# Kernel tuning notes

Hardware: AMD Instinct MI355X
Metric: run time of the kernel (lower is better)

## Reference

```python
import jax, jax.numpy as jnp
import numpy as np

L, B, S, D, H = 4, 4, 2048, 512, 8
DH = D // H
FF = 4 * D
BN_EPS = 1e-3  # keras BatchNormalization default epsilon


def setup_inputs() -> dict:
    key = jax.random.key(0)
    ks = jax.random.split(key, 8)
    g = lambda k, shape: jax.random.normal(k, shape, dtype=jnp.float32) * 0.02
    return {
        "sequence": jax.random.normal(ks[0], (B, S, D), dtype=jnp.float32),
        "wq": g(ks[1], (L, D, D)), "bq": jnp.zeros((L, D), jnp.float32),
        "wk": g(ks[2], (L, D, D)), "bk": jnp.zeros((L, D), jnp.float32),
        "wv": g(ks[3], (L, D, D)), "bv": jnp.zeros((L, D), jnp.float32),
        "wo": g(ks[4], (L, D, D)), "bo": jnp.zeros((L, D), jnp.float32),
        "w1": g(ks[5], (L, D, FF)), "b1": jnp.zeros((L, FF), jnp.float32),
        "w2": g(ks[6], (L, FF, D)), "b2": jnp.zeros((L, D), jnp.float32),
        "g1": jnp.ones((L, D), jnp.float32), "be1": jnp.zeros((L, D), jnp.float32),
        "g2": jnp.ones((L, D), jnp.float32), "be2": jnp.zeros((L, D), jnp.float32),
    }


def reference(sequence, wq, bq, wk, bk, wv, bv, wo, bo, w1, b1, w2, b2, g1, be1, g2, be2):
    # Inference-mode BatchNorm with moving_mean=0, moving_var=1:
    # bn(x) = x / sqrt(1 + eps) * gamma + beta
    bn_inv = 1.0 / jnp.sqrt(jnp.float32(1.0 + BN_EPS))
    scale = 1.0 / jnp.sqrt(jnp.float32(DH))
    x = sequence  # [B, S, D]
    for i in range(L):
        # Batched multi-head self-attention (== the per-position loop concat)
        q = (x @ wq[i] + bq[i]).reshape(B, S, H, DH)
        k = (x @ wk[i] + bk[i]).reshape(B, S, H, DH)
        v = (x @ wv[i] + bv[i]).reshape(B, S, H, DH)
        att = jax.nn.softmax(jnp.einsum('bqhd,bkhd->bhqk', q, k) * scale, axis=-1)
        o = jnp.einsum('bhqk,bkhd->bqhd', att, v).reshape(B, S, D)
        o = o @ wo[i] + bo[i]
        x = (x + o) * bn_inv * g1[i] + be1[i]          # residual + BN
        f = jax.nn.relu(x @ w1[i] + b1[i]) @ w2[i] + b2[i]  # FFN
        x = (x + f) * bn_inv * g2[i] + be2[i]          # residual + BN
    return x
```

## Files before the change

kernel.cpp:

```cpp
#include <hip/hip_runtime.h>
#include <hip/hip_bf16.h>

#define BB   4
#define SS   2048
#define DDIM 512
#define HH   8
#define DHD  64
#define FFD  2048
#define LLN  4
#define NQKV 1536
#define BN_INV 0.9995003747f
#define QSCALE 0.18033688011112042f

typedef __bf16 bf16x8 __attribute__((ext_vector_type(8)));
typedef __bf16 bf16x4 __attribute__((ext_vector_type(4)));
typedef float  f32x4  __attribute__((ext_vector_type(4)));

__device__ __forceinline__ void gl2lds16(const void* g, void* l) {
  __builtin_amdgcn_global_load_lds((const __attribute__((address_space(1))) void*)g,
                                   (__attribute__((address_space(3))) void*)l, 16, 0, 0);
}

__global__ __launch_bounds__(256) void k_transpose_w(const float* __restrict__ in,
                                                     __bf16* __restrict__ out,
                                                     int R, int C,
                                                     size_t in_zs, size_t out_zs) {
  __shared__ float tile[32][33];
  in += (size_t)blockIdx.z * in_zs;
  out += (size_t)blockIdx.z * out_zs;
  const int c0 = blockIdx.x * 32, r0 = blockIdx.y * 32;
  const int tx = threadIdx.x & 31, ty = threadIdx.x >> 5;
#pragma unroll
  for (int k = 0; k < 4; ++k) {
    int r = ty + k * 8;
    tile[r][tx] = in[(size_t)(r0 + r) * C + (c0 + tx)];
  }
  __syncthreads();
#pragma unroll
  for (int k = 0; k < 4; ++k) {
    int c = ty + k * 8;
    out[(size_t)(c0 + c) * R + (r0 + tx)] = (__bf16)tile[tx][c];
  }
}

__global__ __launch_bounds__(256) void k_bias_fuse(const float* __restrict__ bq,
                                                   const float* __restrict__ bk,
                                                   const float* __restrict__ bv,
                                                   float* __restrict__ out) {
  const int i = blockIdx.x * 256 + threadIdx.x;
  const int l = i / NQKV, j = i - l * NQKV;
  float v = (j < 512) ? bq[l * 512 + j]
          : (j < 1024) ? bk[l * 512 + j - 512]
                       : bv[l * 512 + j - 1024];
  out[i] = v;
}

__global__ __launch_bounds__(256) void k_transpose_v(const __bf16* __restrict__ qkv,
                                                     __bf16* __restrict__ vt) {
  __shared__ __bf16 tile[32][33];
  const int s0 = blockIdx.x * 32;
  const int d0 = blockIdx.y * 32;
  const int bh = blockIdx.z, b = bh >> 3, h = bh & 7;
  const int tx = threadIdx.x & 31, ty = threadIdx.x >> 5;
#pragma unroll
  for (int k = 0; k < 4; ++k) {
    int s = ty + k * 8;
    tile[s][tx] = qkv[(size_t)(b * SS + s0 + s) * NQKV + 2 * DDIM + h * DHD + d0 + tx];
  }
  __syncthreads();
#pragma unroll
  for (int k = 0; k < 4; ++k) {
    int d = ty + k * 8;
    vt[(size_t)(bh * DHD + d0 + d) * SS + (s0 + tx)] = tile[tx][d];
  }
}

__global__ __launch_bounds__(256) void k_cast(const float* __restrict__ in,
                                              float* __restrict__ xf,
                                              __bf16* __restrict__ xb) {
  const int i = (blockIdx.x * 256 + threadIdx.x) * 4;
  const float4 v = *(const float4*)(in + i);
  *(float4*)(xf + i) = v;
  bf16x4 o;
  o[0] = (__bf16)v.x; o[1] = (__bf16)v.y; o[2] = (__bf16)v.z; o[3] = (__bf16)v.w;
  *(bf16x4*)(xb + i) = o;
}

template <int EPI>
__global__ __launch_bounds__(256) void k_gemm_bt(const __bf16* __restrict__ A,
                                                 const __bf16* __restrict__ Bt,
                                                 const float* __restrict__ bias,
                                                 __bf16* __restrict__ Cb,
                                                 int M, int N, int K,
                                                 const float* __restrict__ xres,
                                                 float* __restrict__ xout,
                                                 const float* __restrict__ gvec,
                                                 const float* __restrict__ bvec) {
  __shared__ char As[2][16384];
  __shared__ char Bs[2][16384];
  const int tid = threadIdx.x;
  const int l = tid & 63, w = tid >> 6;
  const int wm = w >> 1, wn = w & 1;
  const int m0 = blockIdx.y * 128, n0 = blockIdx.x * 128;
  const int lr = l & 15, lg = l >> 4;
  f32x4 acc[4][4] = {};
  const int nk = K >> 6;
  const size_t ldab = (size_t)K * 2;

  auto stage = [&](int buf, int kt) {
    const int k0b = kt * 128;
#pragma unroll
    for (int i = 0; i < 4; ++i) {
      const int chunk = i * 256 + tid;
      const int row = chunk >> 3;
      const int scb = ((chunk & 7) * 16) ^ ((row & 7) << 4);
      gl2lds16((const char*)A + (size_t)(m0 + row) * ldab + k0b + scb,
               As[buf] + (i * 256 + w * 64) * 16);
      gl2lds16((const char*)Bt + (size_t)(n0 + row) * ldab + k0b + scb,
               Bs[buf] + (i * 256 + w * 64) * 16);
    }
  };

  stage(0, 0);
  __syncthreads();
  int cur = 0;
  for (int kt = 0; kt < nk; ++kt) {
    if (kt + 1 < nk) stage(cur ^ 1, kt + 1);
#pragma unroll
    for (int kk = 0; kk < 2; ++kk) {
      bf16x8 a[4], b[4];
#pragma unroll
      for (int m = 0; m < 4; ++m) {
        const int row = wm * 64 + m * 16 + lr;
        const int cb = kk * 64 + lg * 16;
        a[m] = *(const bf16x8*)(As[cur] + row * 128 + (cb ^ ((row & 7) << 4)));
      }
#pragma unroll
      for (int n = 0; n < 4; ++n) {
        const int row = wn * 64 + n * 16 + lr;
        const int cb = kk * 64 + lg * 16;
        b[n] = *(const bf16x8*)(Bs[cur] + row * 128 + (cb ^ ((row & 7) << 4)));
      }
#pragma unroll
      for (int m = 0; m < 4; ++m)
#pragma unroll
        for (int n = 0; n < 4; ++n)
          acc[m][n] = __builtin_amdgcn_mfma_f32_16x16x32_bf16(a[m], b[n], acc[m][n], 0, 0, 0);
    }
    asm volatile("s_waitcnt vmcnt(0)" ::: "memory");
    __syncthreads();
    cur ^= 1;
  }
#pragma unroll
  for (int m = 0; m < 4; ++m) {
    const int gm = m0 + wm * 64 + m * 16 + lg * 4;
#pragma unroll
    for (int n = 0; n < 4; ++n) {
      const int gn = n0 + wn * 64 + n * 16 + lr;
      const float bv_ = bias[gn];
#pragma unroll
      for (int j = 0; j < 4; ++j) {
        const size_t idx = (size_t)(gm + j) * N + gn;
        float v = acc[m][n][j] + bv_;
        if constexpr (EPI == 1) {
          Cb[idx] = (__bf16)fmaxf(v, 0.0f);
        } else if constexpr (EPI == 2) {
          float t = (xres[idx] + v) * BN_INV * gvec[gn] + bvec[gn];
          xout[idx] = t;
          Cb[idx] = (__bf16)t;
        } else {
          if (gn < DDIM) v *= QSCALE;
          Cb[idx] = (__bf16)v;
        }
      }
    }
  }
}

__global__ __launch_bounds__(512, 4) void k_attn(const __bf16* __restrict__ QKV,
                                                 const __bf16* __restrict__ Vt,
                                                 __bf16* __restrict__ O) {
  __shared__ char smem[81920];
  const int tid = threadIdx.x, l = tid & 63, w = tid >> 6;
  const int lr = l & 15, lg = l >> 4;
  const int f = blockIdx.y * 16 + blockIdx.x;
  const int L = (f & 7) * 64 + (f >> 3);
  const int qt = L & 15, bh = L >> 4;
  const int b = bh >> 3, h = bh & 7;
  const int q0 = qt * 128 + w * 16;
  bf16x8 aq[2];
  {
    const __bf16* qp = QKV + (size_t)(b * SS + q0 + lr) * NQKV + h * DHD + lg * 8;
    aq[0] = *(const bf16x8*)qp;
    aq[1] = *(const bf16x8*)(qp + 32);
  }
  f32x4 oacc[4] = {};
  float rsum[4] = {0.f, 0.f, 0.f, 0.f};
  char* pw = smem + 65536 + w * 2048;

  auto stage = [&](int buf, int t) {
    const int kv0 = t * 128;
    char* Kd = smem + buf * 16384;
    char* Vd = smem + 32768 + buf * 16384;
#pragma unroll
    for (int i = 0; i < 2; ++i) {
      const int chunk = i * 512 + tid;
      const int row = chunk >> 3;
      const int scb = ((chunk & 7) * 16) ^ ((row & 7) << 4);
      gl2lds16((const char*)QKV + ((size_t)(b * SS + kv0 + row) * NQKV + DDIM + h * DHD) * 2 + scb,
               Kd + (i * 512 + w * 64) * 16);
    }
#pragma unroll
    for (int i = 0; i < 2; ++i) {
      const int chunk = i * 512 + tid;
      const int row = chunk >> 4;
      const int scb = ((chunk & 15) * 16) ^ ((row & 7) << 4);
      gl2lds16((const char*)Vt + ((size_t)(bh * DHD + row) * SS + kv0) * 2 + scb,
               Vd + (i * 512 + w * 64) * 16);
    }
  };

  stage(0, 0);
  __syncthreads();
  int cur = 0;
  for (int t = 0; t < SS / 128; ++t) {
    if (t < SS / 128 - 1) stage(cur ^ 1, t + 1);
    const char* Ks = smem + cur * 16384;
    const char* Vs = smem + 32768 + cur * 16384;
    f32x4 s[8];
    __builtin_amdgcn_s_setprio(1);
#pragma unroll
    for (int n = 0; n < 8; ++n) {
      const int row = n * 16 + lr;
      const int swz = (row & 7) << 4;
      bf16x8 kf0 = *(const bf16x8*)(Ks + row * 128 + ((lg * 16) ^ swz));
      bf16x8 kf1 = *(const bf16x8*)(Ks + row * 128 + ((64 + lg * 16) ^ swz));
      f32x4 z = {};
      z = __builtin_amdgcn_mfma_f32_16x16x32_bf16(aq[0], kf0, z, 0, 0, 0);
      z = __builtin_amdgcn_mfma_f32_16x16x32_bf16(aq[1], kf1, z, 0, 0, 0);
      s[n] = z;
    }
    __builtin_amdgcn_s_setprio(0);
#pragma unroll
    for (int hv = 0; hv < 2; ++hv) {
#pragma unroll
      for (int nn = 0; nn < 4; ++nn)
#pragma unroll
        for (int j = 0; j < 4; ++j) {
          const float p = __builtin_amdgcn_exp2f(s[hv * 4 + nn][j]);
          rsum[j] += p;
          const int r = lg * 4 + j;
          const int cb = (nn * 16 + lr) * 2;
          *(__bf16*)(pw + r * 128 + (cb ^ ((r & 7) << 4))) = (__bf16)p;
        }
      __builtin_amdgcn_s_setprio(1);
#pragma unroll
      for (int kk2 = 0; kk2 < 2; ++kk2) {
        const int kkg = hv * 2 + kk2;
        const bf16x8 ap = *(const bf16x8*)(pw + lr * 128 + ((kk2 * 64 + lg * 16) ^ ((lr & 7) << 4)));
#pragma unroll
        for (int n = 0; n < 4; ++n) {
          const int row = n * 16 + lr;
          bf16x8 vf = *(const bf16x8*)(Vs + row * 256 + ((kkg * 64 + lg * 16) ^ ((row & 7) << 4)));
          oacc[n] = __builtin_amdgcn_mfma_f32_16x16x32_bf16(ap, vf, oacc[n], 0, 0, 0);
        }
      }
      __builtin_amdgcn_s_setprio(0);
    }
    asm volatile("s_waitcnt vmcnt(0)" ::: "memory");
    __syncthreads();
    cur ^= 1;
  }
#pragma unroll
  for (int j = 0; j < 4; ++j) {
    float v = rsum[j];
    v += __shfl_xor(v, 1);
    v += __shfl_xor(v, 2);
    v += __shfl_xor(v, 4);
    v += __shfl_xor(v, 8);
    const float inv = 1.0f / v;
    const int sr = q0 + lg * 4 + j;
#pragma unroll
    for (int n = 0; n < 4; ++n)
      O[(size_t)(b * SS + sr) * DDIM + h * DHD + n * 16 + lr] = (__bf16)(oacc[n][j] * inv);
  }
}

static constexpr size_t SZ_WQKVT = (size_t)LLN * NQKV * DDIM * 2;
static constexpr size_t SZ_WOT   = (size_t)LLN * DDIM * DDIM * 2;
static constexpr size_t SZ_WT_DF = (size_t)LLN * DDIM * FFD * 2;
static constexpr size_t SZ_BQKV  = (size_t)LLN * NQKV * 4;
static constexpr size_t SZ_X     = (size_t)BB * SS * DDIM * 4;
static constexpr size_t SZ_ABF   = (size_t)BB * SS * DDIM * 2;
static constexpr size_t SZ_QKV   = (size_t)BB * SS * NQKV * 2;
static constexpr size_t OFF_WQKVT = 0;
static constexpr size_t OFF_WOT  = OFF_WQKVT + SZ_WQKVT;
static constexpr size_t OFF_W1T  = OFF_WOT + SZ_WOT;
static constexpr size_t OFF_W2T  = OFF_W1T + SZ_WT_DF;
static constexpr size_t OFF_BQKV = OFF_W2T + SZ_WT_DF;
static constexpr size_t OFF_X    = OFF_BQKV + SZ_BQKV;
static constexpr size_t OFF_XB   = OFF_X + SZ_X;
static constexpr size_t OFF_QKV  = OFF_XB + SZ_ABF;
static constexpr size_t OFF_VT   = OFF_QKV + SZ_QKV;
static constexpr size_t OFF_OB   = OFF_VT + SZ_ABF;
static constexpr size_t OFF_H1   = OFF_QKV;

extern "C" void kernel_launch(void* const* d_in, const int* in_sizes, int n_in,
                              void* d_out, int out_size, void* d_ws, size_t ws_size,
                              hipStream_t stream) {
  const float* seq = (const float*)d_in[0];
  const float* wq = (const float*)d_in[1];  const float* bq = (const float*)d_in[2];
  const float* wk = (const float*)d_in[3];  const float* bk = (const float*)d_in[4];
  const float* wv = (const float*)d_in[5];  const float* bv = (const float*)d_in[6];
  const float* wo = (const float*)d_in[7];  const float* bo = (const float*)d_in[8];
  const float* w1 = (const float*)d_in[9];  const float* b1 = (const float*)d_in[10];
  const float* w2 = (const float*)d_in[11]; const float* b2 = (const float*)d_in[12];
  const float* g1 = (const float*)d_in[13]; const float* be1 = (const float*)d_in[14];
  const float* g2 = (const float*)d_in[15]; const float* be2 = (const float*)d_in[16];

  char* ws = (char*)d_ws;
  __bf16* wqkvt = (__bf16*)(ws + OFF_WQKVT);
  __bf16* wot = (__bf16*)(ws + OFF_WOT);
  __bf16* w1t = (__bf16*)(ws + OFF_W1T);
  __bf16* w2t = (__bf16*)(ws + OFF_W2T);
  float*  bqkv = (float*)(ws + OFF_BQKV);
  float*  xf  = (float*)(ws + OFF_X);
  __bf16* xb  = (__bf16*)(ws + OFF_XB);
  __bf16* qkvb = (__bf16*)(ws + OFF_QKV);
  __bf16* vtb = (__bf16*)(ws + OFF_VT);
  __bf16* ob  = (__bf16*)(ws + OFF_OB);
  __bf16* h1  = (__bf16*)(ws + OFF_H1);

  const size_t zDD = (size_t)DDIM * DDIM;
  const size_t zQKV = (size_t)NQKV * DDIM;
  const size_t zDF = (size_t)DDIM * FFD;
  k_transpose_w<<<dim3(16, 16, LLN), 256, 0, stream>>>(wq, wqkvt, DDIM, DDIM, zDD, zQKV);
  k_transpose_w<<<dim3(16, 16, LLN), 256, 0, stream>>>(wk, wqkvt + (size_t)DDIM * DDIM, DDIM, DDIM, zDD, zQKV);
  k_transpose_w<<<dim3(16, 16, LLN), 256, 0, stream>>>(wv, wqkvt + (size_t)2 * DDIM * DDIM, DDIM, DDIM, zDD, zQKV);
  k_transpose_w<<<dim3(16, 16, LLN), 256, 0, stream>>>(wo, wot, DDIM, DDIM, zDD, zDD);
  k_transpose_w<<<dim3(64, 16, LLN), 256, 0, stream>>>(w1, w1t, DDIM, FFD, zDF, zDF);
  k_transpose_w<<<dim3(16, 64, LLN), 256, 0, stream>>>(w2, w2t, FFD, DDIM, zDF, zDF);
  k_bias_fuse<<<LLN * NQKV / 256, 256, 0, stream>>>(bq, bk, bv, bqkv);
  k_cast<<<4096, 256, 0, stream>>>(seq, xf, xb);

  const int M = BB * SS;
  for (int i = 0; i < LLN; ++i) {
    k_gemm_bt<3><<<dim3(NQKV / 128, M / 128), 256, 0, stream>>>(
        xb, wqkvt + (size_t)i * NQKV * DDIM, bqkv + i * NQKV, qkvb, M, NQKV, DDIM,
        nullptr, nullptr, nullptr, nullptr);
    k_transpose_v<<<dim3(SS / 32, DHD / 32, BB * HH), 256, 0, stream>>>(qkvb, vtb);
    k_attn<<<dim3(SS / 128, BB * HH), 512, 0, stream>>>(qkvb, vtb, ob);
    k_gemm_bt<2><<<dim3(DDIM / 128, M / 128), 256, 0, stream>>>(
        ob, wot + (size_t)i * DDIM * DDIM, bo + i * DDIM, xb, M, DDIM, DDIM,
        xf, xf, g1 + i * DDIM, be1 + i * DDIM);
    k_gemm_bt<1><<<dim3(FFD / 128, M / 128), 256, 0, stream>>>(
        xb, w1t + (size_t)i * DDIM * FFD, b1 + i * FFD, h1, M, FFD, DDIM,
        nullptr, nullptr, nullptr, nullptr);
    k_gemm_bt<2><<<dim3(DDIM / 128, M / 128), 256, 0, stream>>>(
        h1, w2t + (size_t)i * DDIM * FFD, b2 + i * DDIM, xb, M, DDIM, FFD,
        xf, (i == LLN - 1) ? (float*)d_out : xf, g2 + i * DDIM, be2 + i * DDIM);
  }
  (void)in_sizes; (void)n_in; (void)out_size; (void)ws_size;
}
```

Before: 677.1 us.

## Restructure attention to 32x32 MFMA computing S^T so P stays in registers

Rewrites the attention kernel to use 32x32x16 bf16 MFMAs with 4 waves of 32 query rows each, computing the transposed score tile so that the exponentiated probabilities land directly in the B-operand layout for the PV MFMA. This removes the per-wave LDS round trip for P, along with its shared memory and barriers, and shrinks the block to 256 threads. K rows are permuted during staging and the V swizzle is widened to match the new fragment layout. The risks are lower occupancy from fewer waves per block and higher register pressure from the 16-wide accumulators, plus the correctness of the new row permutation.

Measured after the change: 642.5 us. 5.1% less time.

```diff
diff --git a/kernel.cpp b/kernel.cpp
--- a/kernel.cpp
+++ b/kernel.cpp
@@ -15,10 +15,17 @@
 typedef __bf16 bf16x8 __attribute__((ext_vector_type(8)));
 typedef __bf16 bf16x4 __attribute__((ext_vector_type(4)));
 typedef float  f32x4  __attribute__((ext_vector_type(4)));
+typedef float  f32x16 __attribute__((ext_vector_type(16)));
 
 __device__ __forceinline__ void gl2lds16(const void* g, void* l) {
   __builtin_amdgcn_global_load_lds((const __attribute__((address_space(1))) void*)g,
                                    (__attribute__((address_space(3))) void*)l, 16, 0, 0);
+}
+
+__device__ __forceinline__ unsigned pkbf16(float a, float b) {
+  union { __bf16 h[2]; unsigned u; } x;
+  x.h[0] = (__bf16)a; x.h[1] = (__bf16)b;
+  return x.u;
 }
 
 __global__ __launch_bounds__(256) void k_transpose_w(const float* __restrict__ in,
@@ -177,46 +184,47 @@
   }
 }
 
-__global__ __launch_bounds__(512, 4) void k_attn(const __bf16* __restrict__ QKV,
+__global__ __launch_bounds__(256, 2) void k_attn(const __bf16* __restrict__ QKV,
                                                  const __bf16* __restrict__ Vt,
                                                  __bf16* __restrict__ O) {
-  __shared__ char smem[81920];
+  __shared__ char smem[65536];
   const int tid = threadIdx.x, l = tid & 63, w = tid >> 6;
-  const int lr = l & 15, lg = l >> 4;
+  const int lq = l & 31, hi = l >> 5;
   const int f = blockIdx.y * 16 + blockIdx.x;
   const int L = (f & 7) * 64 + (f >> 3);
   const int qt = L & 15, bh = L >> 4;
   const int b = bh >> 3, h = bh & 7;
-  const int q0 = qt * 128 + w * 16;
-  bf16x8 aq[2];
+  const int myq = qt * 128 + w * 32 + lq;
+  bf16x8 qf[4];
   {
-    const __bf16* qp = QKV + (size_t)(b * SS + q0 + lr) * NQKV + h * DHD + lg * 8;
-    aq[0] = *(const bf16x8*)qp;
-    aq[1] = *(const bf16x8*)(qp + 32);
-  }
-  f32x4 oacc[4] = {};
-  float rsum[4] = {0.f, 0.f, 0.f, 0.f};
-  char* pw = smem + 65536 + w * 2048;
+    const __bf16* qp = QKV + (size_t)(b * SS + myq) * NQKV + h * DHD + hi * 8;
+#pragma unroll
+    for (int kc = 0; kc < 4; ++kc)
+      qf[kc] = *(const bf16x8*)(qp + kc * 16);
+  }
+  f32x16 oaccT[2] = {};
+  float rsum = 0.f;
 
   auto stage = [&](int buf, int t) {
     const int kv0 = t * 128;
     char* Kd = smem + buf * 16384;
     char* Vd = smem + 32768 + buf * 16384;
 #pragma unroll
-    for (int i = 0; i < 2; ++i) {
-      const int chunk = i * 512 + tid;
+    for (int i = 0; i < 4; ++i) {
+      const int chunk = i * 256 + tid;
       const int row = chunk >> 3;
+      const int rs = row ^ ((((row >> 2) + 1) & 2) * 6);
       const int scb = ((chunk & 7) * 16) ^ ((row & 7) << 4);
-      gl2lds16((const char*)QKV + ((size_t)(b * SS + kv0 + row) * NQKV + DDIM + h * DHD) * 2 + scb,
-               Kd + (i * 512 + w * 64) * 16);
-    }
-#pragma unroll
-    for (int i = 0; i < 2; ++i) {
-      const int chunk = i * 512 + tid;
+      gl2lds16((const char*)QKV + ((size_t)(b * SS + kv0 + rs) * NQKV + DDIM + h * DHD) * 2 + scb,
+               Kd + (i * 256 + w * 64) * 16);
+    }
+#pragma unroll
+    for (int i = 0; i < 4; ++i) {
+      const int chunk = i * 256 + tid;
       const int row = chunk >> 4;
-      const int scb = ((chunk & 15) * 16) ^ ((row & 7) << 4);
+      const int scb = ((chunk & 15) * 16) ^ ((row & 15) << 4);
       gl2lds16((const char*)Vt + ((size_t)(bh * DHD + row) * SS + kv0) * 2 + scb,
-               Vd + (i * 512 + w * 64) * 16);
+               Vd + (i * 256 + w * 64) * 16);
     }
   };
 
@@ -227,43 +235,38 @@
     if (t < SS / 128 - 1) stage(cur ^ 1, t + 1);
     const char* Ks = smem + cur * 16384;
     const char* Vs = smem + 32768 + cur * 16384;
-    f32x4 s[8];
-    __builtin_amdgcn_s_setprio(1);
-#pragma unroll
-    for (int n = 0; n < 8; ++n) {
-      const int row = n * 16 + lr;
-      const int swz = (row & 7) << 4;
-      bf16x8 kf0 = *(const bf16x8*)(Ks + row * 128 + ((lg * 16) ^ swz));
-      bf16x8 kf1 = *(const bf16x8*)(Ks + row * 128 + ((64 + lg * 16) ^ swz));
-      f32x4 z = {};
-      z = __builtin_amdgcn_mfma_f32_16x16x32_bf16(aq[0], kf0, z, 0, 0, 0);
-      z = __builtin_amdgcn_mfma_f32_16x16x32_bf16(aq[1], kf1, z, 0, 0, 0);
-      s[n] = z;
-    }
-    __builtin_amdgcn_s_setprio(0);
-#pragma unroll
-    for (int hv = 0; hv < 2; ++hv) {
-#pragma unroll
-      for (int nn = 0; nn < 4; ++nn)
-#pragma unroll
-        for (int j = 0; j < 4; ++j) {
-          const float p = __builtin_amdgcn_exp2f(s[hv * 4 + nn][j]);
-          rsum[j] += p;
-          const int r = lg * 4 + j;
-          const int cb = (nn * 16 + lr) * 2;
-          *(__bf16*)(pw + r * 128 + (cb ^ ((r & 7) << 4))) = (__bf16)p;
-        }
+#pragma unroll
+    for (int kt2 = 0; kt2 < 4; ++kt2) {
+      const int krow = kt2 * 32 + lq;
+      const int kswz = (krow & 7) << 4;
+      f32x16 st = {};
       __builtin_amdgcn_s_setprio(1);
 #pragma unroll
-      for (int kk2 = 0; kk2 < 2; ++kk2) {
-        const int kkg = hv * 2 + kk2;
-        const bf16x8 ap = *(const bf16x8*)(pw + lr * 128 + ((kk2 * 64 + lg * 16) ^ ((lr & 7) << 4)));
-#pragma unroll
-        for (int n = 0; n < 4; ++n) {
-          const int row = n * 16 + lr;
-          bf16x8 vf = *(const bf16x8*)(Vs + row * 256 + ((kkg * 64 + lg * 16) ^ ((row & 7) << 4)));
-          oacc[n] = __builtin_amdgcn_mfma_f32_16x16x32_bf16(ap, vf, oacc[n], 0, 0, 0);
-        }
+      for (int kc = 0; kc < 4; ++kc) {
+        bf16x8 kf = *(const bf16x8*)(Ks + krow * 128 + ((kc * 32 + hi * 16) ^ kswz));
+        st = __builtin_amdgcn_mfma_f32_32x32x16_bf16(kf, qf[kc], st, 0, 0, 0);
+      }
+      __builtin_amdgcn_s_setprio(0);
+      unsigned pk8[8];
+#pragma unroll
+      for (int i = 0; i < 8; ++i) {
+        const float e0 = __builtin_amdgcn_exp2f(st[2 * i]);
+        const float e1 = __builtin_amdgcn_exp2f(st[2 * i + 1]);
+        rsum += e0 + e1;
+        pk8[i] = pkbf16(e0, e1);
+      }
+      union { unsigned u[4]; bf16x8 v; } pf0, pf1;
+#pragma unroll
+      for (int i = 0; i < 4; ++i) { pf0.u[i] = pk8[i]; pf1.u[i] = pk8[4 + i]; }
+      __builtin_amdgcn_s_setprio(1);
+#pragma unroll
+      for (int dt = 0; dt < 2; ++dt) {
+        const int vrow = dt * 32 + lq;
+        const int vswz = (vrow & 15) << 4;
+        bf16x8 vf0 = *(const bf16x8*)(Vs + vrow * 256 + ((kt2 * 64 + hi * 16) ^ vswz));
+        bf16x8 vf1 = *(const bf16x8*)(Vs + vrow * 256 + ((kt2 * 64 + 32 + hi * 16) ^ vswz));
+        oaccT[dt] = __builtin_amdgcn_mfma_f32_32x32x16_bf16(vf0, pf0.v, oaccT[dt], 0, 0, 0);
+        oaccT[dt] = __builtin_amdgcn_mfma_f32_32x32x16_bf16(vf1, pf1.v, oaccT[dt], 0, 0, 0);
       }
       __builtin_amdgcn_s_setprio(0);
     }
@@ -271,19 +274,19 @@
     __syncthreads();
     cur ^= 1;
   }
-#pragma unroll
-  for (int j = 0; j < 4; ++j) {
-    float v = rsum[j];
-    v += __shfl_xor(v, 1);
-    v += __shfl_xor(v, 2);
-    v += __shfl_xor(v, 4);
-    v += __shfl_xor(v, 8);
-    const float inv = 1.0f / v;
-    const int sr = q0 + lg * 4 + j;
-#pragma unroll
-    for (int n = 0; n < 4; ++n)
-      O[(size_t)(b * SS + sr) * DDIM + h * DHD + n * 16 + lr] = (__bf16)(oacc[n][j] * inv);
-  }
+  rsum += __shfl_xor(rsum, 32);
+  const float inv = 1.0f / rsum;
+  __bf16* op = O + (size_t)(b * SS + myq) * DDIM + h * DHD;
+#pragma unroll
+  for (int dt = 0; dt < 2; ++dt)
+#pragma unroll
+    for (int g = 0; g < 4; ++g) {
+      const int d0 = dt * 32 + g * 8 + hi * 4;
+      unsigned u0 = pkbf16(oaccT[dt][4 * g + 0] * inv, oaccT[dt][4 * g + 1] * inv);
+      unsigned u1 = pkbf16(oaccT[dt][4 * g + 2] * inv, oaccT[dt][4 * g + 3] * inv);
+      uint2 uu; uu.x = u0; uu.y = u1;
+      *(uint2*)(op + d0) = uu;
+    }
 }
 
 static constexpr size_t SZ_WQKVT = (size_t)LLN * NQKV * DDIM * 2;
@@ -349,7 +352,7 @@
         xb, wqkvt + (size_t)i * NQKV * DDIM, bqkv + i * NQKV, qkvb, M, NQKV, DDIM,
         nullptr, nullptr, nullptr, nullptr);
     k_transpose_v<<<dim3(SS / 32, DHD / 32, BB * HH), 256, 0, stream>>>(qkvb, vtb);
-    k_attn<<<dim3(SS / 128, BB * HH), 512, 0, stream>>>(qkvb, vtb, ob);
+    k_attn<<<dim3(SS / 128, BB * HH), 256, 0, stream>>>(qkvb, vtb, ob);
     k_gemm_bt<2><<<dim3(DDIM / 128, M / 128), 256, 0, stream>>>(
         ob, wot + (size_t)i * DDIM * DDIM, bo + i * DDIM, xb, M, DDIM, DDIM,
         xf, xf, g1 + i * DDIM, be1 + i * DDIM);
```
